# Performance work log

Hardware: AMD Instinct MI355X
Metric: run time of the kernel (lower is better)

The kernel has to match this reference:

```python
import jax, jax.numpy as jnp
import numpy as np

N_NODE = 100_000
N_EDGE = 2_000_000
IN_DIM = 64
OUT_DIM = 64
ATTN_DIM = 32
N_REL = 200   # rela_embed has 2*N_REL+1 = 401 rows
N_ENT = 50_000
BATCH = 8


def setup_inputs() -> dict:
    key = jax.random.key(0)
    ks = jax.random.split(key, 16)
    # edges columns: 0=r_idx (query index in batch), 2=rel, 4=sub, 5=obj; cols 1,3 unused
    r_idx = jax.random.randint(ks[0], (N_EDGE,), 0, BATCH, dtype=jnp.int32)
    rel = jax.random.randint(ks[1], (N_EDGE,), 0, 2 * N_REL + 1, dtype=jnp.int32)
    sub = jax.random.randint(ks[2], (N_EDGE,), 0, N_NODE, dtype=jnp.int32)
    obj = jax.random.randint(ks[3], (N_EDGE,), 0, N_NODE, dtype=jnp.int32)
    pad = jnp.zeros((N_EDGE,), jnp.int32)
    edges = jnp.stack([r_idx, pad, rel, pad, sub, obj], axis=1)
    nodes = jnp.stack(
        [jax.random.randint(ks[4], (N_NODE,), 0, BATCH, dtype=jnp.int32),
         jax.random.randint(ks[5], (N_NODE,), 0, N_ENT, dtype=jnp.int32)], axis=1)
    s = 0.05
    return {
        "q_sub": jax.random.randint(ks[6], (BATCH,), 0, N_ENT, dtype=jnp.int32),
        "q_rel": jax.random.randint(ks[7], (BATCH,), 0, 2 * N_REL + 1, dtype=jnp.int32),
        "hidden": jax.random.normal(ks[8], (N_NODE, IN_DIM), jnp.float32),
        "edges": edges,
        "nodes": nodes,
        "old_nodes_new_idx": jnp.arange(N_NODE // 2, dtype=jnp.int32),
        "batchsize": BATCH,
        "rela_embed": jax.random.normal(ks[9], (2 * N_REL + 1, IN_DIM), jnp.float32) * s,
        "Ws": jax.random.normal(ks[10], (ATTN_DIM, IN_DIM), jnp.float32) * s,
        "Wr": jax.random.normal(ks[11], (ATTN_DIM, IN_DIM), jnp.float32) * s,
        "Wqr": jax.random.normal(ks[12], (ATTN_DIM, IN_DIM), jnp.float32) * s,
        "bqr": jax.random.normal(ks[13], (ATTN_DIM,), jnp.float32) * s,
        "w_alpha_w": jax.random.normal(ks[14], (1, ATTN_DIM), jnp.float32) * s,
        "w_alpha_b": jnp.zeros((1,), jnp.float32),
        "Wh": jax.random.normal(ks[15], (OUT_DIM, IN_DIM), jnp.float32) * s,
    }


def reference(q_sub, q_rel, hidden, edges, nodes, old_nodes_new_idx, batchsize,
              rela_embed, Ws, Wr, Wqr, bqr, w_alpha_w, w_alpha_b, Wh):
    sub = edges[:, 4]
    rel = edges[:, 2]
    obj = edges[:, 5]
    r_idx = edges[:, 0]
    n_node = hidden.shape[0]

    hs = hidden[sub]                      # [E, in_dim] gather
    hr = rela_embed[rel]                  # [E, in_dim] gather
    h_qr = rela_embed[q_rel][r_idx]       # [E, in_dim] gather of per-query rel embed

    # attention: sigmoid(w_alpha(relu(Ws hs + Wr hr + Wqr h_qr + bqr)))
    attn = jax.nn.relu(hs @ Ws.T + hr @ Wr.T + h_qr @ Wqr.T + bqr)  # [E, attn_dim]
    alpha = jax.nn.sigmoid(attn @ w_alpha_w.T + w_alpha_b)           # [E, 1]

    message = alpha * (hs + hr)           # [E, in_dim]
    message_agg = jax.ops.segment_sum(message, obj, num_segments=n_node)  # [n_node, in_dim]
    hidden_new = message_agg @ Wh.T       # act is identity (default)
    return hidden_new
```

## Files before the change

### kernel.cpp

```cpp
#include <hip/hip_runtime.h>
#include <hip/hip_bf16.h>


typedef __attribute__((ext_vector_type(8))) short bf16x8;
typedef __attribute__((ext_vector_type(4))) float f32x4;

__device__ inline unsigned short f2bf(float x) {
    unsigned u = __float_as_uint(x);
    u += 0x7FFF + ((u >> 16) & 1);
    return (unsigned short)(u >> 16);
}
__device__ inline float bf2f(unsigned short b) {
    return __uint_as_float(((unsigned)b) << 16);
}

__device__ inline bf16x8 pack8(float4 a, float4 b) {
    bf16x8 r;
    r[0] = (short)f2bf(a.x); r[1] = (short)f2bf(a.y);
    r[2] = (short)f2bf(a.z); r[3] = (short)f2bf(a.w);
    r[4] = (short)f2bf(b.x); r[5] = (short)f2bf(b.y);
    r[6] = (short)f2bf(b.z); r[7] = (short)f2bf(b.w);
    return r;
}

template<int NT>
__global__ void proj_mfma_kernel(const float* __restrict__ X, const float* __restrict__ W,
                                 unsigned short* __restrict__ out, int nrows) {
    int lane = threadIdx.x & 63;
    int wv   = threadIdx.x >> 6;
    int m0   = (blockIdx.x * 4 + wv) * 16;
    if (m0 >= nrows) return;
    int lr = lane & 15;
    int lk = lane >> 4;

    bf16x8 bfr[NT][2];
#pragma unroll
    for (int nt = 0; nt < NT; ++nt)
#pragma unroll
        for (int ks = 0; ks < 2; ++ks) {
            const float* wp = W + (size_t)(nt * 16 + lr) * 64 + ks * 32 + lk * 8;
            float4 w0 = *(const float4*)wp;
            float4 w1 = *(const float4*)(wp + 4);
            bfr[nt][ks] = pack8(w0, w1);
        }

    int row = m0 + lr;
    if (row >= nrows) row = nrows - 1;
    const float* xp = X + (size_t)row * 64 + lk * 8;
    float4 x0 = *(const float4*)xp;
    float4 x1 = *(const float4*)(xp + 4);
    float4 x2 = *(const float4*)(xp + 32);
    float4 x3 = *(const float4*)(xp + 36);
    bf16x8 a0 = pack8(x0, x1);
    bf16x8 a1 = pack8(x2, x3);

    f32x4 acc[NT];
#pragma unroll
    for (int nt = 0; nt < NT; ++nt) {
        acc[nt] = (f32x4){0.f, 0.f, 0.f, 0.f};
        acc[nt] = __builtin_amdgcn_mfma_f32_16x16x32_bf16(a0, bfr[nt][0], acc[nt], 0, 0, 0);
        acc[nt] = __builtin_amdgcn_mfma_f32_16x16x32_bf16(a1, bfr[nt][1], acc[nt], 0, 0, 0);
    }

#pragma unroll
    for (int nt = 0; nt < NT; ++nt)
#pragma unroll
        for (int r = 0; r < 4; ++r) {
            int ro = m0 + lk * 4 + r;
            if (ro < nrows)
                out[(size_t)ro * (NT * 16) + nt * 16 + lr] = f2bf(acc[nt][r]);
        }
}

__global__ void qproj_bf16_kernel(const int* __restrict__ q_rel, const float* __restrict__ rela,
                                  const float* __restrict__ Wqr, const float* __restrict__ bqr,
                                  unsigned* __restrict__ Qb, int batch) {
    int tid = threadIdx.x;
    int b = tid >> 5, k = tid & 31;
    if (b >= batch) return;
    int qr = q_rel[b];
    const float* x = rela + (size_t)qr * 64;
    const float* w = Wqr + (size_t)k * 64;
    float acc = bqr[k];
    for (int d = 0; d < 64; ++d) acc += w[d] * x[d];
    float other = __shfl_xor(acc, 1, 64);
    if ((k & 1) == 0) {
        unsigned lo = f2bf(acc), hi = f2bf(other);
        Qb[b * 16 + (k >> 1)] = lo | (hi << 16);
    }
}

__global__ void pack_hist_kernel(const int4* __restrict__ edges4, int2* __restrict__ pk2,
                                 int* __restrict__ hmat, int n_edge, int NB) {
    __shared__ int hist[256];
    int tid = threadIdx.x, blk = blockIdx.x;
    hist[tid] = 0;
    __syncthreads();
    int unit0 = blk * 2048;
#pragma unroll
    for (int k = 0; k < 8; ++k) {
        int u = unit0 + k * 256 + tid;
        int base = u * 4;
        if (base >= n_edge) break;
        if (base + 4 <= n_edge) {
            const int4* p = edges4 + (size_t)u * 6;
            int4 v0 = p[0], v1 = p[1], v2 = p[2], v3 = p[3], v4 = p[4], v5 = p[5];
            atomicAdd(&hist[v1.y >> 9], 1);
            atomicAdd(&hist[v2.w >> 9], 1);
            atomicAdd(&hist[v4.y >> 9], 1);
            atomicAdd(&hist[v5.w >> 9], 1);
            int4 o0, o1;
            o0.x = v1.x | (v0.z << 17); o0.y = v1.y | (v0.x << 17);
            o0.z = v2.z | (v2.x << 17); o0.w = v2.w | (v1.z << 17);
            o1.x = v4.x | (v3.z << 17); o1.y = v4.y | (v3.x << 17);
            o1.z = v5.z | (v5.x << 17); o1.w = v5.w | (v4.z << 17);
            int4* q = (int4*)pk2 + (size_t)u * 2;
            q[0] = o0;
            q[1] = o1;
        } else {
            const int* ei = (const int*)edges4;
            for (int e = base; e < n_edge; ++e) {
                const int* ep = ei + (size_t)e * 6;
                int ridx = ep[0], rel = ep[2], sub = ep[4], obj = ep[5];
                atomicAdd(&hist[obj >> 9], 1);
                pk2[e] = make_int2(sub | (rel << 17), obj | (ridx << 17));
            }
        }
    }
    __syncthreads();
    hmat[tid * NB + blk] = hist[tid];
}

#define SCAN_CHUNK 1024

__global__ void scan_partial_kernel(const int* __restrict__ counts, int* __restrict__ bsum,
                                    int N) {
    __shared__ int s[256];
    int base = blockIdx.x * SCAN_CHUNK;
    int tid = threadIdx.x;
    int sum = 0;
#pragma unroll
    for (int k = 0; k < 4; ++k) {
        int idx = base + k * 256 + tid;
        if (idx < N) sum += counts[idx];
    }
    s[tid] = sum;
    __syncthreads();
    for (int off = 128; off > 0; off >>= 1) {
        if (tid < off) s[tid] += s[tid + off];
        __syncthreads();
    }
    if (tid == 0) bsum[blockIdx.x] = s[0];
}

__global__ void scan_bsum_kernel(int* __restrict__ bsum, int* __restrict__ offs, int B, int N) {
    __shared__ int s[1024];
    int tid = threadIdx.x;
    int v = (tid < B) ? bsum[tid] : 0;
    s[tid] = v;
    __syncthreads();
    for (int off = 1; off < 1024; off <<= 1) {
        int t = (tid >= off) ? s[tid - off] : 0;
        __syncthreads();
        s[tid] += t;
        __syncthreads();
    }
    if (tid < B) bsum[tid] = s[tid] - v;
    if (tid == 0) offs[N] = s[1023];
}

__global__ void scan_final_kernel(const int* __restrict__ counts, const int* __restrict__ bsum,
                                  int* __restrict__ offs, int N) {
    __shared__ int s[256];
    int base = blockIdx.x * SCAN_CHUNK;
    int tid = threadIdx.x;
    int v[4];
    int sum = 0;
#pragma unroll
    for (int k = 0; k < 4; ++k) {
        int idx = base + tid * 4 + k;
        v[k] = (idx < N) ? counts[idx] : 0;
        sum += v[k];
    }
    s[tid] = sum;
    __syncthreads();
    for (int off = 1; off < 256; off <<= 1) {
        int t = (tid >= off) ? s[tid - off] : 0;
        __syncthreads();
        s[tid] += t;
        __syncthreads();
    }
    int run = bsum[blockIdx.x] + s[tid] - sum;
#pragma unroll
    for (int k = 0; k < 4; ++k) {
        int idx = base + tid * 4 + k;
        if (idx < N) offs[idx] = run;
        run += v[k];
    }
}

__global__ void scatter1_kernel(const int2* __restrict__ pk2, const int* __restrict__ hscan,
                                int2* __restrict__ outrec, int n_edge, int NB) {
    __shared__ int cur[256];
    int tid = threadIdx.x, blk = blockIdx.x;
    cur[tid] = hscan[tid * NB + blk];
    __syncthreads();
    int unit0 = blk * 2048;
#pragma unroll
    for (int k = 0; k < 8; ++k) {
        int u = unit0 + k * 256 + tid;
        int base = u * 4;
        if (base >= n_edge) break;
        if (base + 4 <= n_edge) {
            const int4* q = (const int4*)pk2 + (size_t)u * 2;
            int4 a = q[0], b = q[1];
            int p0 = atomicAdd(&cur[(a.y >> 9) & 0xFF], 1);
            int p1 = atomicAdd(&cur[(a.w >> 9) & 0xFF], 1);
            int p2 = atomicAdd(&cur[(b.y >> 9) & 0xFF], 1);
            int p3 = atomicAdd(&cur[(b.w >> 9) & 0xFF], 1);
            outrec[p0] = make_int2(a.x, a.y);
            outrec[p1] = make_int2(a.z, a.w);
            outrec[p2] = make_int2(b.x, b.y);
            outrec[p3] = make_int2(b.z, b.w);
        } else {
            for (int e = base; e < n_edge; ++e) {
                int2 r = pk2[e];
                int p = atomicAdd(&cur[(r.y >> 9) & 0xFF], 1);
                outrec[p] = r;
            }
        }
    }
}

#define BS_CAP 12288
__global__ __launch_bounds__(512) void bucket_sort_kernel(const int2* __restrict__ in,
                                                          const int* __restrict__ hscan,
                                                          int2* __restrict__ out,
                                                          int* __restrict__ counts,
                                                          int NB, int n_node) {
    __shared__ int hist[512];
    __shared__ int sbase[512];
    __shared__ int cur[512];
    __shared__ int2 st[BS_CAP];
    int b = blockIdx.x, tid = threadIdx.x;
    int start = hscan[b * NB];
    int end   = hscan[(b + 1) * NB];
    int size  = end - start;
    hist[tid] = 0;
    __syncthreads();
    bool inlds = (size <= BS_CAP);
    if (inlds) {
        for (int i = tid; i < size; i += 512) {
            int2 v = in[start + i];
            st[i] = v;
            atomicAdd(&hist[v.y & 511], 1);
        }
    } else {
        for (int i = tid; i < size; i += 512) {
            int2 v = in[start + i];
            atomicAdd(&hist[v.y & 511], 1);
        }
    }
    __syncthreads();
    int obj = (b << 9) | tid;
    int h = hist[tid];
    if (obj < n_node) counts[obj] = h;
    sbase[tid] = h;
    __syncthreads();
    for (int off = 1; off < 512; off <<= 1) {
        int t = (tid >= off) ? sbase[tid - off] : 0;
        __syncthreads();
        sbase[tid] += t;
        __syncthreads();
    }
    cur[tid] = sbase[tid] - h;
    __syncthreads();
    if (inlds) {
        for (int i = tid; i < size; i += 512) {
            int2 r = st[i];
            int p = atomicAdd(&cur[r.y & 511], 1);
            out[start + p] = r;
        }
    } else {
        for (int i = tid; i < size; i += 512) {
            int2 r = in[start + i];
            int p = atomicAdd(&cur[r.y & 511], 1);
            out[start + p] = r;
        }
    }
}

__device__ inline float edot(unsigned sv, unsigned rv, unsigned qv, float2 w) {
    float a0 = fmaxf(bf2f((unsigned short)sv) + bf2f((unsigned short)rv)
                     + bf2f((unsigned short)qv), 0.f);
    float a1 = fmaxf(bf2f((unsigned short)(sv >> 16)) + bf2f((unsigned short)(rv >> 16))
                     + bf2f((unsigned short)(qv >> 16)), 0.f);
    return a0 * w.x + a1 * w.y;
}

__global__ void alpha_kernel(const int2* __restrict__ pk2,
                             const unsigned* __restrict__ Sb,
                             const unsigned* __restrict__ Rb,
                             const unsigned* __restrict__ Qb,
                             const float2* __restrict__ w2,
                             const float* __restrict__ w_alpha_b,
                             float2* __restrict__ rec,
                             int n_edge) {
    int tid = threadIdx.x;
    int lane = tid & 15;
    int e0 = (blockIdx.x * 16 + (tid >> 4)) * 4;
    if (e0 >= n_edge) return;
    int eN = n_edge - 1;
    int2 h0 = pk2[e0];
    int2 h1 = pk2[min(e0 + 1, eN)];
    int2 h2 = pk2[min(e0 + 2, eN)];
    int2 h3 = pk2[min(e0 + 3, eN)];
    float2 w = w2[lane];
    unsigned sv0 = Sb[(size_t)(h0.x & 0x1FFFF) * 16 + lane];
    unsigned sv1 = Sb[(size_t)(h1.x & 0x1FFFF) * 16 + lane];
    unsigned sv2 = Sb[(size_t)(h2.x & 0x1FFFF) * 16 + lane];
    unsigned sv3 = Sb[(size_t)(h3.x & 0x1FFFF) * 16 + lane];
    unsigned rv0 = Rb[(size_t)(h0.x >> 17) * 16 + lane];
    unsigned rv1 = Rb[(size_t)(h1.x >> 17) * 16 + lane];
    unsigned rv2 = Rb[(size_t)(h2.x >> 17) * 16 + lane];
    unsigned rv3 = Rb[(size_t)(h3.x >> 17) * 16 + lane];
    unsigned qv0 = Qb[((h0.y >> 17) & 7) * 16 + lane];
    unsigned qv1 = Qb[((h1.y >> 17) & 7) * 16 + lane];
    unsigned qv2 = Qb[((h2.y >> 17) & 7) * 16 + lane];
    unsigned qv3 = Qb[((h3.y >> 17) & 7) * 16 + lane];
    float p0 = edot(sv0, rv0, qv0, w);
    float p1 = edot(sv1, rv1, qv1, w);
    float p2 = edot(sv2, rv2, qv2, w);
    float p3 = edot(sv3, rv3, qv3, w);
#pragma unroll
    for (int off = 8; off > 0; off >>= 1) {
        p0 += __shfl_xor(p0, off, 16);
        p1 += __shfl_xor(p1, off, 16);
        p2 += __shfl_xor(p2, off, 16);
        p3 += __shfl_xor(p3, off, 16);
    }
    if (lane < 4 && e0 + lane < n_edge) {
        float p = p0; int2 h = h0;
        if (lane == 1) { p = p1; h = h1; }
        if (lane == 2) { p = p2; h = h2; }
        if (lane == 3) { p = p3; h = h3; }
        float alpha = 1.f / (1.f + __expf(-(p + w_alpha_b[0])));
        float2 out;
        out.x = alpha;
        out.y = __int_as_float(h.x);
        rec[e0 + lane] = out;
    }
}

__global__ void reduce_kernel(const float2* __restrict__ rec, const int* __restrict__ offs,
                              const ushort4* __restrict__ Hw4,
                              const ushort4* __restrict__ Rw4,
                              float4* __restrict__ out4, int n_node) {
    int lane = threadIdx.x & 63;
    int node = blockIdx.x * 4 + (threadIdx.x >> 6);
    if (node >= n_node) return;
    int g = lane >> 4;
    int t = lane & 15;
    int start = offs[node], end = offs[node + 1];
    float4 acc = make_float4(0.f, 0.f, 0.f, 0.f);

    for (int i = start; i < end; i += 64) {
        int m = end - i;
        if (m > 64) m = 64;
        float a = 0.f;
        int pk = 0;
        if (lane < m) {
            float2 r = rec[i + lane];
            a = r.x;
            pk = __float_as_int(r.y);
        }
        int nj = (m + 3) >> 2;

        float A0, A1, A2, A3;
        ushort4 H0, H1, H2, H3, R0, R1, R2, R3;

#define RD_ISSUE(S, J) do {                                                   \
        int src_ = 4 * (J) + g;                                               \
        bool ok_ = (src_ < m);                                                \
        int s_ = ok_ ? src_ : 0;                                              \
        float a_ = __shfl(a, s_, 64);                                         \
        int p_ = __shfl(pk, s_, 64);                                          \
        A##S = ok_ ? a_ : 0.f;                                                \
        int sub_ = p_ & 0x1FFFF, rel_ = p_ >> 17;                             \
        H##S = Hw4[(size_t)sub_ * 16 + t];                                    \
        R##S = Rw4[(size_t)rel_ * 16 + t];                                    \
    } while (0)

#define RD_CONSUME(S) do {                                                    \
        acc.x += A##S * (bf2f(H##S.x) + bf2f(R##S.x));                        \
        acc.y += A##S * (bf2f(H##S.y) + bf2f(R##S.y));                        \
        acc.z += A##S * (bf2f(H##S.z) + bf2f(R##S.z));                        \
        acc.w += A##S * (bf2f(H##S.w) + bf2f(R##S.w));                        \
    } while (0)

        RD_ISSUE(0, 0);
        RD_ISSUE(1, 1);
        RD_ISSUE(2, 2);
        RD_ISSUE(3, 3);
        for (int j = 0; j < nj; j += 4) {
            RD_CONSUME(0); RD_ISSUE(0, j + 4);
            RD_CONSUME(1); RD_ISSUE(1, j + 5);
            RD_CONSUME(2); RD_ISSUE(2, j + 6);
            RD_CONSUME(3); RD_ISSUE(3, j + 7);
        }
#undef RD_ISSUE
#undef RD_CONSUME
    }
#pragma unroll
    for (int off = 16; off <= 32; off <<= 1) {
        acc.x += __shfl_xor(acc.x, off, 64);
        acc.y += __shfl_xor(acc.y, off, 64);
        acc.z += __shfl_xor(acc.z, off, 64);
        acc.w += __shfl_xor(acc.w, off, 64);
    }
    if (g == 0) out4[(size_t)node * 16 + t] = acc;
}

extern "C" void kernel_launch(void* const* d_in, const int* in_sizes, int n_in,
                              void* d_out, int out_size, void* d_ws, size_t ws_size,
                              hipStream_t stream) {
    const int*   q_rel     = (const int*)d_in[1];
    const float* hidden    = (const float*)d_in[2];
    const int*   edges     = (const int*)d_in[3];
    const float* rela      = (const float*)d_in[7];
    const float* Ws        = (const float*)d_in[8];
    const float* Wr        = (const float*)d_in[9];
    const float* Wqr       = (const float*)d_in[10];
    const float* bqr       = (const float*)d_in[11];
    const float* w_alpha_w = (const float*)d_in[12];
    const float* w_alpha_b = (const float*)d_in[13];
    const float* Wh        = (const float*)d_in[14];

    int n_node = in_sizes[2] / 64;
    int n_edge = in_sizes[3] / 6;
    int n_rel  = in_sizes[7] / 64;
    int batch  = in_sizes[1];

    int NB = (n_edge + 8191) / 8192;
    int N2 = NB * 256;
    int n_sblk  = (n_node + SCAN_CHUNK - 1) / SCAN_CHUNK;
    int n_sblk2 = (N2 + SCAN_CHUNK - 1) / SCAN_CHUNK;

    unsigned* Sb   = (unsigned*)d_ws;
    unsigned* Rb   = Sb + (size_t)n_node * 16;
    unsigned* Qb   = Rb + (size_t)n_rel * 16;
    int*   counts  = (int*)(Qb + (size_t)batch * 16);
    int*   offs    = counts + n_node;
    int*   bsum    = offs + n_node + 1;
    int*   hmat    = bsum + 1024;
    int*   hscan   = hmat + N2;
    size_t rec_off = (size_t)(hscan + N2 + 1 - (int*)d_ws);
    rec_off = (rec_off + 3) & ~(size_t)3;
    float2* rec    = (float2*)((int*)d_ws + rec_off);
    int2*  pk2     = (int2*)(rec + n_edge);
    unsigned short* Hw = (unsigned short*)pk2;
    unsigned short* Rw = Hw + (size_t)n_node * 64;

    proj_mfma_kernel<2><<<(n_node + 63) / 64, 256, 0, stream>>>(
        hidden, Ws, (unsigned short*)Sb, n_node);
    proj_mfma_kernel<2><<<(n_rel + 63) / 64, 256, 0, stream>>>(
        rela, Wr, (unsigned short*)Rb, n_rel);
    qproj_bf16_kernel<<<1, 256, 0, stream>>>(q_rel, rela, Wqr, bqr, Qb, batch);

    pack_hist_kernel<<<NB, 256, 0, stream>>>((const int4*)edges, pk2, hmat, n_edge, NB);

    scan_partial_kernel<<<n_sblk2, 256, 0, stream>>>(hmat, bsum, N2);
    scan_bsum_kernel<<<1, 1024, 0, stream>>>(bsum, hscan, n_sblk2, N2);
    scan_final_kernel<<<n_sblk2, 256, 0, stream>>>(hmat, bsum, hscan, N2);

    scatter1_kernel<<<NB, 256, 0, stream>>>(pk2, hscan, (int2*)rec, n_edge, NB);
    bucket_sort_kernel<<<256, 512, 0, stream>>>((const int2*)rec, hscan, pk2, counts,
                                                NB, n_node);

    scan_partial_kernel<<<n_sblk, 256, 0, stream>>>(counts, bsum, n_node);
    scan_bsum_kernel<<<1, 1024, 0, stream>>>(bsum, offs, n_sblk, n_node);
    scan_final_kernel<<<n_sblk, 256, 0, stream>>>(counts, bsum, offs, n_node);

    alpha_kernel<<<(n_edge + 63) / 64, 256, 0, stream>>>(
        pk2, Sb, Rb, Qb, (const float2*)w_alpha_w, w_alpha_b, rec, n_edge);

    proj_mfma_kernel<4><<<(n_node + 63) / 64, 256, 0, stream>>>(hidden, Wh, Hw, n_node);
    proj_mfma_kernel<4><<<(n_rel + 63) / 64, 256, 0, stream>>>(rela, Wh, Rw, n_rel);

    reduce_kernel<<<(n_node + 3) / 4, 256, 0, stream>>>(
        rec, offs, (const ushort4*)Hw, (const ushort4*)Rw, (float4*)d_out, n_node);
}
```

Baseline: 324.2 us.

## Compute CSR offsets in bucket sort, use fp16 packed math in reduce

Bucket sort now writes the per-node CSR offsets straight from its in-block prefix scan, which removes the separate counts array and three scan kernels. The Wh projections are stored as fp16, and the reduce kernel accumulates with packed half2 FMAs instead of converting bf16 to fp32 per element. Record loads and output stores become nontemporal. Accumulating in fp16 risks precision loss and overflow on high-degree nodes. The offset write relies on the bucket layout mapping node n_node to the end of the edge array.

```diff
diff --git a/kernel.cpp b/kernel.cpp
--- a/kernel.cpp
+++ b/kernel.cpp
@@ -1,9 +1,11 @@
 #include <hip/hip_runtime.h>
 #include <hip/hip_bf16.h>
+#include <hip/hip_fp16.h>
 
 
 typedef __attribute__((ext_vector_type(8))) short bf16x8;
 typedef __attribute__((ext_vector_type(4))) float f32x4;
+typedef __attribute__((ext_vector_type(2))) float f32x2;
 
 __device__ inline unsigned short f2bf(float x) {
     unsigned u = __float_as_uint(x);
@@ -12,6 +14,9 @@
 }
 __device__ inline float bf2f(unsigned short b) {
     return __uint_as_float(((unsigned)b) << 16);
+}
+__device__ inline __half2 u2h2(unsigned u) {
+    return __builtin_bit_cast(__half2, u);
 }
 
 __device__ inline bf16x8 pack8(float4 a, float4 b) {
@@ -23,7 +28,7 @@
     return r;
 }
 
-template<int NT>
+template<int NT, bool F16>
 __global__ void proj_mfma_kernel(const float* __restrict__ X, const float* __restrict__ W,
                                  unsigned short* __restrict__ out, int nrows) {
     int lane = threadIdx.x & 63;
@@ -67,8 +72,16 @@
 #pragma unroll
         for (int r = 0; r < 4; ++r) {
             int ro = m0 + lk * 4 + r;
-            if (ro < nrows)
-                out[(size_t)ro * (NT * 16) + nt * 16 + lr] = f2bf(acc[nt][r]);
+            if (ro < nrows) {
+                unsigned short bits;
+                if (F16) {
+                    __half h = __float2half(acc[nt][r]);
+                    bits = __builtin_bit_cast(unsigned short, h);
+                } else {
+                    bits = f2bf(acc[nt][r]);
+                }
+                out[(size_t)ro * (NT * 16) + nt * 16 + lr] = bits;
+            }
         }
 }
 
@@ -236,7 +249,7 @@
 __global__ __launch_bounds__(512) void bucket_sort_kernel(const int2* __restrict__ in,
                                                           const int* __restrict__ hscan,
                                                           int2* __restrict__ out,
-                                                          int* __restrict__ counts,
+                                                          int* __restrict__ offs,
                                                           int NB, int n_node) {
     __shared__ int hist[512];
     __shared__ int sbase[512];
@@ -262,9 +275,7 @@
         }
     }
     __syncthreads();
-    int obj = (b << 9) | tid;
     int h = hist[tid];
-    if (obj < n_node) counts[obj] = h;
     sbase[tid] = h;
     __syncthreads();
     for (int off = 1; off < 512; off <<= 1) {
@@ -273,7 +284,10 @@
         sbase[tid] += t;
         __syncthreads();
     }
-    cur[tid] = sbase[tid] - h;
+    int ebase = sbase[tid] - h;
+    cur[tid] = ebase;
+    int obj = (b << 9) | tid;
+    if (obj <= n_node) offs[obj] = start + ebase;
     __syncthreads();
     if (inlds) {
         for (int i = tid; i < size; i += 512) {
@@ -353,8 +367,8 @@
 }
 
 __global__ void reduce_kernel(const float2* __restrict__ rec, const int* __restrict__ offs,
-                              const ushort4* __restrict__ Hw4,
-                              const ushort4* __restrict__ Rw4,
+                              const uint2* __restrict__ Hw2,
+                              const uint2* __restrict__ Rw2,
                               float4* __restrict__ out4, int n_node) {
     int lane = threadIdx.x & 63;
     int node = blockIdx.x * 4 + (threadIdx.x >> 6);
@@ -362,7 +376,8 @@
     int g = lane >> 4;
     int t = lane & 15;
     int start = offs[node], end = offs[node + 1];
-    float4 acc = make_float4(0.f, 0.f, 0.f, 0.f);
+    __half2 acc0 = __float2half2_rn(0.f);
+    __half2 acc1 = __float2half2_rn(0.f);
 
     for (int i = start; i < end; i += 64) {
         int m = end - i;
@@ -370,14 +385,14 @@
         float a = 0.f;
         int pk = 0;
         if (lane < m) {
-            float2 r = rec[i + lane];
+            f32x2 r = __builtin_nontemporal_load((const f32x2*)&rec[i + lane]);
             a = r.x;
             pk = __float_as_int(r.y);
         }
         int nj = (m + 3) >> 2;
 
-        float A0, A1, A2, A3;
-        ushort4 H0, H1, H2, H3, R0, R1, R2, R3;
+        __half2 A0, A1, A2, A3;
+        uint2 H0, H1, H2, H3, R0, R1, R2, R3;
 
 #define RD_ISSUE(S, J) do {                                                   \
         int src_ = 4 * (J) + g;                                               \
@@ -385,17 +400,15 @@
         int s_ = ok_ ? src_ : 0;                                              \
         float a_ = __shfl(a, s_, 64);                                         \
         int p_ = __shfl(pk, s_, 64);                                          \
-        A##S = ok_ ? a_ : 0.f;                                                \
+        A##S = __float2half2_rn(ok_ ? a_ : 0.f);                              \
         int sub_ = p_ & 0x1FFFF, rel_ = p_ >> 17;                             \
-        H##S = Hw4[(size_t)sub_ * 16 + t];                                    \
-        R##S = Rw4[(size_t)rel_ * 16 + t];                                    \
+        H##S = Hw2[(size_t)sub_ * 16 + t];                                    \
+        R##S = Rw2[(size_t)rel_ * 16 + t];                                    \
     } while (0)
 
 #define RD_CONSUME(S) do {                                                    \
-        acc.x += A##S * (bf2f(H##S.x) + bf2f(R##S.x));                        \
-        acc.y += A##S * (bf2f(H##S.y) + bf2f(R##S.y));                        \
-        acc.z += A##S * (bf2f(H##S.z) + bf2f(R##S.z));                        \
-        acc.w += A##S * (bf2f(H##S.w) + bf2f(R##S.w));                        \
+        acc0 = __hfma2(A##S, __hadd2(u2h2(H##S.x), u2h2(R##S.x)), acc0);      \
+        acc1 = __hfma2(A##S, __hadd2(u2h2(H##S.y), u2h2(R##S.y)), acc1);      \
     } while (0)
 
         RD_ISSUE(0, 0);
@@ -411,6 +424,9 @@
 #undef RD_ISSUE
 #undef RD_CONSUME
     }
+    float2 f0 = __half22float2(acc0);
+    float2 f1 = __half22float2(acc1);
+    f32x4 acc = (f32x4){f0.x, f0.y, f1.x, f1.y};
 #pragma unroll
     for (int off = 16; off <= 32; off <<= 1) {
         acc.x += __shfl_xor(acc.x, off, 64);
@@ -418,7 +434,8 @@
         acc.z += __shfl_xor(acc.z, off, 64);
         acc.w += __shfl_xor(acc.w, off, 64);
     }
-    if (g == 0) out4[(size_t)node * 16 + t] = acc;
+    if (g == 0)
+        __builtin_nontemporal_store(acc, (f32x4*)&out4[(size_t)node * 16 + t]);
 }
 
 extern "C" void kernel_launch(void* const* d_in, const int* in_sizes, int n_in,
@@ -443,14 +460,12 @@
 
     int NB = (n_edge + 8191) / 8192;
     int N2 = NB * 256;
-    int n_sblk  = (n_node + SCAN_CHUNK - 1) / SCAN_CHUNK;
     int n_sblk2 = (N2 + SCAN_CHUNK - 1) / SCAN_CHUNK;
 
     unsigned* Sb   = (unsigned*)d_ws;
     unsigned* Rb   = Sb + (size_t)n_node * 16;
     unsigned* Qb   = Rb + (size_t)n_rel * 16;
-    int*   counts  = (int*)(Qb + (size_t)batch * 16);
-    int*   offs    = counts + n_node;
+    int*   offs    = (int*)(Qb + (size_t)batch * 16);
     int*   bsum    = offs + n_node + 1;
     int*   hmat    = bsum + 1024;
     int*   hscan   = hmat + N2;
@@ -461,9 +476,9 @@
     unsigned short* Hw = (unsigned short*)pk2;
     unsigned short* Rw = Hw + (size_t)n_node * 64;
 
-    proj_mfma_kernel<2><<<(n_node + 63) / 64, 256, 0, stream>>>(
+    proj_mfma_kernel<2, false><<<(n_node + 63) / 64, 256, 0, stream>>>(
         hidden, Ws, (unsigned short*)Sb, n_node);
-    proj_mfma_kernel<2><<<(n_rel + 63) / 64, 256, 0, stream>>>(
+    proj_mfma_kernel<2, false><<<(n_rel + 63) / 64, 256, 0, stream>>>(
         rela, Wr, (unsigned short*)Rb, n_rel);
     qproj_bf16_kernel<<<1, 256, 0, stream>>>(q_rel, rela, Wqr, bqr, Qb, batch);
 
@@ -474,19 +489,15 @@
     scan_final_kernel<<<n_sblk2, 256, 0, stream>>>(hmat, bsum, hscan, N2);
 
     scatter1_kernel<<<NB, 256, 0, stream>>>(pk2, hscan, (int2*)rec, n_edge, NB);
-    bucket_sort_kernel<<<256, 512, 0, stream>>>((const int2*)rec, hscan, pk2, counts,
+    bucket_sort_kernel<<<256, 512, 0, stream>>>((const int2*)rec, hscan, pk2, offs,
                                                 NB, n_node);
-
-    scan_partial_kernel<<<n_sblk, 256, 0, stream>>>(counts, bsum, n_node);
-    scan_bsum_kernel<<<1, 1024, 0, stream>>>(bsum, offs, n_sblk, n_node);
-    scan_final_kernel<<<n_sblk, 256, 0, stream>>>(counts, bsum, offs, n_node);
 
     alpha_kernel<<<(n_edge + 63) / 64, 256, 0, stream>>>(
         pk2, Sb, Rb, Qb, (const float2*)w_alpha_w, w_alpha_b, rec, n_edge);
 
-    proj_mfma_kernel<4><<<(n_node + 63) / 64, 256, 0, stream>>>(hidden, Wh, Hw, n_node);
-    proj_mfma_kernel<4><<<(n_rel + 63) / 64, 256, 0, stream>>>(rela, Wh, Rw, n_rel);
+    proj_mfma_kernel<4, true><<<(n_node + 63) / 64, 256, 0, stream>>>(hidden, Wh, Hw, n_node);
+    proj_mfma_kernel<4, true><<<(n_rel + 63) / 64, 256, 0, stream>>>(rela, Wh, Rw, n_rel);
 
     reduce_kernel<<<(n_node + 3) / 4, 256, 0, stream>>>(
-        rec, offs, (const ushort4*)Hw, (const ushort4*)Rw, (float4*)d_out, n_node);
-}
+        rec, offs, (const uint2*)Hw, (const uint2*)Rw, (float4*)d_out, n_node);
+}
```

After: 316.4 us. 1.02x faster.
